# Kernel optimization log

Measured on AMD Instinct MI355X. Metric: run time of the kernel, lower is better.

The kernel has to match this reference:

```python
import jax, jax.numpy as jnp
import numpy as np

PC_RANGE = (-50.0, -50.0, -4.0, 50.0, 50.0, 4.0)
IMG_H, IMG_W = 256.0, 704.0
EPS = 1e-5


def _bilinear_sample(feat, u, v):
    # feat [H,W,C]; u,v [M] in [0,1]; matches F.grid_sample(align_corners=False, padding_mode='zeros')
    H, W, _ = feat.shape
    x = u * W - 0.5
    y = v * H - 0.5
    x0 = jnp.floor(x)
    y0 = jnp.floor(y)
    dx = (x - x0)[:, None]
    dy = (y - y0)[:, None]
    x0 = x0.astype(jnp.int32)
    y0 = y0.astype(jnp.int32)

    def g(xi, yi):
        inb = ((xi >= 0) & (xi < W) & (yi >= 0) & (yi < H)).astype(feat.dtype)[:, None]
        return feat[jnp.clip(yi, 0, H - 1), jnp.clip(xi, 0, W - 1)] * inb

    return (g(x0, y0) * (1 - dx) * (1 - dy) + g(x0 + 1, y0) * dx * (1 - dy)
            + g(x0, y0 + 1) * (1 - dx) * dy + g(x0 + 1, y0 + 1) * dx * dy)


def _conv1x1(t, w, b):
    return jnp.einsum('bchw,oc->bohw', t, w) + b[None, :, None, None]


def _inorm(t, eps=1e-5):
    # InstanceNorm2d (affine=False): normalize per (b, c) over spatial dims
    m = t.mean(axis=(2, 3), keepdims=True)
    var = t.var(axis=(2, 3), keepdims=True)
    return (t - m) * jax.lax.rsqrt(var + eps)


def _forward(feat, lidar2img, bev_pos, pe_w1, pe_b1, pe_w2, pe_b2, pe_w3, pe_b3,
             c1_w, c1_b, c2_w, c2_b, c3_w, c3_b):
    B, N, C, Hf, Wf = feat.shape
    _, P, Hb, Wb, _ = bev_pos.shape
    Q = Hb * Wb
    lo = jnp.asarray(PC_RANGE[:3], feat.dtype)
    hi = jnp.asarray(PC_RANGE[3:], feat.dtype)
    # 'b p h w d -> b (h w) p d', then scale normalized coords into pc_range
    ref01 = jnp.transpose(bev_pos, (0, 2, 3, 1, 4)).reshape(B, Q, P, 3)
    ref = ref01 * (hi - lo) + lo
    # project through per-camera lidar2img (homogeneous)
    pts = jnp.concatenate([ref, jnp.ones_like(ref[..., :1])], axis=-1)  # [B,Q,P,4]
    cam = jnp.einsum('bnij,bqpj->bnqpi', lidar2img, pts)                # [B,N,Q,P,4]
    homo = cam[..., 2]
    z = jnp.maximum(homo, EPS)
    u = cam[..., 0] / z / IMG_W
    v = cam[..., 1] / z / IMG_H
    valid = ((homo > EPS) & (u > 0.0) & (u < 1.0) & (v > 0.0) & (v < 1.0)).astype(feat.dtype)
    # bilinear gather per camera; feats to channel-last ('b n (g c) h w -> (b g) n h w c', G=1)
    fmap = jnp.transpose(feat, (0, 1, 3, 4, 2)).reshape(B * N, Hf, Wf, C)
    samp = jax.vmap(_bilinear_sample)(fmap, u.reshape(B * N, Q * P), v.reshape(B * N, Q * P))
    samp = samp.reshape(B, N, Q, P, C) * valid[..., None]
    samp = samp.sum(axis=1)  # sum over cameras -> [B,Q,P,C]
    # PositionalEncodingMap(3 -> 256 -> 256 -> 128) on normalized reference points
    pe = jax.nn.relu(ref01 @ pe_w1 + pe_b1)
    pe = jax.nn.relu(pe @ pe_w2 + pe_b2)
    pe = pe @ pe_w3 + pe_b3
    samp = samp + pe
    # 'b (h w) g p c -> b (p g c) h w' with g=1
    x = jnp.transpose(samp.reshape(B, Hb, Wb, P, C), (0, 3, 4, 1, 2)).reshape(B, P * C, Hb, Wb)
    gelu = lambda t: jax.nn.gelu(t, approximate=False)
    x = gelu(_inorm(_conv1x1(x, c1_w, c1_b)))
    x = gelu(_inorm(_conv1x1(x, c2_w, c2_b)))
    x = _conv1x1(x, c3_w, c3_b)
    return x


def setup_inputs() -> dict:
    key = jax.random.key(0)
    ks = jax.random.split(key, 16)
    B, N, C, Hf, Wf = 1, 6, 128, 32, 88
    P, Hb, Wb = 4, 160, 160
    E = 128
    MID = 256
    s = 0.02
    return {
        'feat': jax.random.normal(ks[0], (B, N, C, Hf, Wf), jnp.float32),
        'lidar2img': jax.random.normal(ks[1], (B, N, 4, 4), jnp.float32),
        'bev_pos': jax.random.uniform(ks[2], (B, P, Hb, Wb, 3), jnp.float32),
        'pe_w1': jax.random.normal(ks[3], (3, MID), jnp.float32) * s,
        'pe_b1': jnp.zeros((MID,), jnp.float32),
        'pe_w2': jax.random.normal(ks[4], (MID, MID), jnp.float32) * s,
        'pe_b2': jnp.zeros((MID,), jnp.float32),
        'pe_w3': jax.random.normal(ks[5], (MID, E), jnp.float32) * s,
        'pe_b3': jnp.zeros((E,), jnp.float32),
        'c1_w': jax.random.normal(ks[6], (4 * E, P * 128), jnp.float32) * s,
        'c1_b': jnp.zeros((4 * E,), jnp.float32),
        'c2_w': jax.random.normal(ks[7], (E, 4 * E), jnp.float32) * s,
        'c2_b': jnp.zeros((E,), jnp.float32),
        'c3_w': jax.random.normal(ks[8], (E, E), jnp.float32) * s,
        'c3_b': jnp.zeros((E,), jnp.float32),
    }


def reference(feat, lidar2img, bev_pos, pe_w1, pe_b1, pe_w2, pe_b2, pe_w3, pe_b3,
              c1_w, c1_b, c2_w, c2_b, c3_w, c3_b):
    return _forward(feat, lidar2img, bev_pos, pe_w1, pe_b1, pe_w2, pe_b2, pe_w3, pe_b3,
                    c1_w, c1_b, c2_w, c2_b, c3_w, c3_b)
```

## Files before the change

### kernel.cpp

```cpp
#include <hip/hip_runtime.h>
#include <cstdint>
#include <cstddef>

using frag8 = __attribute__((ext_vector_type(8))) short;
using f32x4 = __attribute__((ext_vector_type(4))) float;

__device__ __forceinline__ float b2f_bits(unsigned short u) {
    union { uint32_t u32; float f; } x; x.u32 = ((uint32_t)u) << 16; return x.f;
}
__device__ __forceinline__ float b2f_lo(uint32_t pk) {
    return __builtin_bit_cast(float, pk << 16);
}
__device__ __forceinline__ float b2f_hi(uint32_t pk) {
    return __builtin_bit_cast(float, pk & 0xffff0000u);
}
__device__ __forceinline__ unsigned short f2b(float f) {
    uint32_t u = __builtin_bit_cast(uint32_t, f);
    uint32_t r = (u + 0x7fffu + ((u >> 16) & 1u)) >> 16;
    return (unsigned short)r;
}

#define HF 32
#define WFEAT 88
#define NCAM 6
#define NPT 102400
#define BM 128
#define BN 128
#define BK 64

__global__ void k_transpose_feat(const float* __restrict__ feat,
                                 unsigned short* __restrict__ featT) {
    int idx = blockIdx.x * 256 + threadIdx.x;
    if (idx >= NCAM * 128 * HF * WFEAT) return;
    int c = idx & 127;
    int rest = idx >> 7;
    int x = rest % WFEAT; rest /= WFEAT;
    int y = rest % HF;
    int n = rest / HF;
    featT[idx] = f2b(feat[((n * 128 + c) * HF + y) * WFEAT + x]);
}

__global__ void k_transpose_w(const float* __restrict__ w,
                              unsigned short* __restrict__ wt, int R, int C) {
    int idx = blockIdx.x * 256 + threadIdx.x;
    if (idx >= R * C) return;
    int r = idx / C, c = idx - r * C;
    wt[c * R + r] = f2b(w[idx]);
}

__global__ void k_cast(const float* __restrict__ w, unsigned short* __restrict__ wb, int n) {
    int idx = blockIdx.x * 256 + threadIdx.x;
    if (idx < n) wb[idx] = f2b(w[idx]);
}

__global__ __launch_bounds__(256) void k_project(const float* __restrict__ l2i,
                                                 const float* __restrict__ bev,
                                                 int* __restrict__ poff,
                                                 float4* __restrict__ pwts) {
    int idx = blockIdx.x * 256 + threadIdx.x;
    if (idx >= NCAM * NPT) return;
    int n = idx / NPT, pt = idx - n * NPT;
    int q = pt >> 2, p = pt & 3;
    int h = q / 160, w = q - h * 160;
    const float* bv = bev + ((p * 160 + h) * 160 + w) * 3;
    float rx = bv[0] * 100.f - 50.f;
    float ry = bv[1] * 100.f - 50.f;
    float rz = bv[2] * 8.f - 4.f;
    const float* M = l2i + n * 16;
    float c0   = M[0] * rx + M[1] * ry + M[2]  * rz + M[3];
    float c1v  = M[4] * rx + M[5] * ry + M[6]  * rz + M[7];
    float homo = M[8] * rx + M[9] * ry + M[10] * rz + M[11];
    float z = fmaxf(homo, 1e-5f);
    float u = c0 / z / 704.0f;
    float v = c1v / z / 256.0f;
    if (!(homo > 1e-5f && u > 0.f && u < 1.f && v > 0.f && v < 1.f)) {
        poff[idx] = -1;
        return;
    }
    float fx = u * (float)WFEAT - 0.5f;
    float fy = v * (float)HF - 0.5f;
    float fx0 = floorf(fx), fy0 = floorf(fy);
    float dx = fx - fx0, dy = fy - fy0;
    int x0 = (int)fx0, y0 = (int)fy0;
    float wxa = (x0 < 0) ? dx : 1.f - dx;
    float wxb = (x0 >= 0 && x0 < WFEAT - 1) ? dx : 0.f;
    float wya = (y0 < 0) ? dy : 1.f - dy;
    float wyb = (y0 >= 0 && y0 < HF - 1) ? dy : 0.f;
    int bx = max(x0, 0), by = max(y0, 0);
    poff[idx] = ((n * HF + by) * WFEAT + bx) << 7;
    pwts[idx] = make_float4(wxa * wya, wxb * wya, wxa * wyb, wxb * wyb);
}

__global__ __launch_bounds__(256) void k_sample2(const unsigned short* __restrict__ featT,
                                                 const int* __restrict__ poff,
                                                 const float4* __restrict__ pwts,
                                                 unsigned short* __restrict__ samp) {
    int pt = blockIdx.x * 4 + (threadIdx.x >> 6);
    int lane = threadIdx.x & 63;
    int c2 = lane * 2;
    int offs[NCAM];
    float4 ww[NCAM];
    #pragma unroll
    for (int n = 0; n < NCAM; ++n) offs[n] = poff[n * NPT + pt];
    #pragma unroll
    for (int n = 0; n < NCAM; ++n) ww[n] = pwts[n * NPT + pt];
    float acc0 = 0.f, acc1 = 0.f;
    #pragma unroll
    for (int n = 0; n < NCAM; ++n) {
        if (offs[n] >= 0) {
            const unsigned short* base = featT + offs[n] + c2;
            uint32_t p00 = *(const uint32_t*)(base);
            uint32_t p01 = *(const uint32_t*)(base + 128);
            uint32_t p10 = *(const uint32_t*)(base + WFEAT * 128);
            uint32_t p11 = *(const uint32_t*)(base + WFEAT * 128 + 128);
            float4 w = ww[n];
            acc0 += w.x * b2f_lo(p00) + w.y * b2f_lo(p01) + w.z * b2f_lo(p10) + w.w * b2f_lo(p11);
            acc1 += w.x * b2f_hi(p00) + w.y * b2f_hi(p01) + w.z * b2f_hi(p10) + w.w * b2f_hi(p11);
        }
    }
    uint32_t outpk = (uint32_t)f2b(acc0) | ((uint32_t)f2b(acc1) << 16);
    *(uint32_t*)(samp + (size_t)pt * 128 + c2) = outpk;
}

__global__ __launch_bounds__(256) void k_pe1(const float* __restrict__ bev,
                                             const float* __restrict__ w1,
                                             const float* __restrict__ b1,
                                             unsigned short* __restrict__ H1) {
    int idx = blockIdx.x * 256 + threadIdx.x;
    int m = idx >> 6;
    int o4 = (idx & 63) * 4;
    int q = m >> 2, p = m & 3;
    int h = q / 160, w = q - h * 160;
    const float* bv = bev + ((p * 160 + h) * 160 + w) * 3;
    float cx = bv[0], cy = bv[1], cz = bv[2];
    float4 a0 = *(const float4*)(w1 + o4);
    float4 a1 = *(const float4*)(w1 + 256 + o4);
    float4 a2 = *(const float4*)(w1 + 512 + o4);
    float4 bb = *(const float4*)(b1 + o4);
    ushort4 o;
    o.x = f2b(fmaxf(cx * a0.x + cy * a1.x + cz * a2.x + bb.x, 0.f));
    o.y = f2b(fmaxf(cx * a0.y + cy * a1.y + cz * a2.y + bb.y, 0.f));
    o.z = f2b(fmaxf(cx * a0.z + cy * a1.z + cz * a2.z + bb.z, 0.f));
    o.w = f2b(fmaxf(cx * a0.w + cy * a1.w + cz * a2.w + bb.w, 0.f));
    *(ushort4*)(H1 + (size_t)m * 256 + o4) = o;
}

__device__ __forceinline__ void stage_tile_big(const unsigned short* __restrict__ g, int ld,
                                               unsigned short* lds, int t) {
    int r = t >> 2, cs = t & 3;
    int cl = cs ^ ((r >> 1) & 3);
    __builtin_amdgcn_global_load_lds(
        (const __attribute__((address_space(1))) void*)(g + (size_t)r * ld + cl * 8),
        (__attribute__((address_space(3))) void*)(lds + (t >> 6) * 512),
        16, 0, 0);
}

__device__ __forceinline__ frag8 frag_read_big(const unsigned short* lds, int row, int chunk) {
    return *(const frag8*)(lds + row * 32 + ((chunk ^ ((row >> 1) & 3)) << 3));
}

__device__ __forceinline__ void mma_tile_big(const unsigned short* As, const unsigned short* Bs,
                                             int wm, int wn, int lane, f32x4 (&acc)[4][4]) {
    int lm = lane & 15, lq = lane >> 4;
    frag8 a[4], b[4];
    #pragma unroll
    for (int t = 0; t < 4; ++t) a[t] = frag_read_big(As, wm * 64 + t * 16 + lm, lq);
    #pragma unroll
    for (int t = 0; t < 4; ++t) b[t] = frag_read_big(Bs, wn * 64 + t * 16 + lm, lq);
    #pragma unroll
    for (int tm = 0; tm < 4; ++tm)
        #pragma unroll
        for (int tn = 0; tn < 4; ++tn)
            acc[tm][tn] = __builtin_amdgcn_mfma_f32_16x16x32_bf16(a[tm], b[tn], acc[tm][tn], 0, 0, 0);
}

template <int KT>
__device__ __forceinline__ void gemm_loop_big(const unsigned short* __restrict__ A, int ldA,
                                              const unsigned short* __restrict__ B, int ldB,
                                              unsigned short (*As)[256 * 32],
                                              unsigned short (*Bs)[256 * 32],
                                              int t, int wm, int wn, int lane,
                                              f32x4 (&acc)[4][4]) {
    stage_tile_big(A, ldA, As[0], t);
    stage_tile_big(B, ldB, Bs[0], t);
    __syncthreads();
    #pragma unroll
    for (int kt = 0; kt < KT; ++kt) {
        int cur = kt & 1, nxt = cur ^ 1;
        if (kt + 1 < KT) {
            stage_tile_big(A + (kt + 1) * 32, ldA, As[nxt], t);
            stage_tile_big(B + (kt + 1) * 32, ldB, Bs[nxt], t);
        }
        mma_tile_big(As[cur], Bs[cur], wm, wn, lane, acc);
        __syncthreads();
    }
}

__global__ __launch_bounds__(1024) void k_gemm_pe2_big(const unsigned short* __restrict__ A,
                                                       const unsigned short* __restrict__ Bt,
                                                       const float* __restrict__ bias,
                                                       unsigned short* __restrict__ H2) {
    __shared__ unsigned short As[2][256 * 32], Bs[2][256 * 32];
    int t = threadIdx.x, lane = t & 63, wid = t >> 6;
    int wm = wid >> 2, wn = wid & 3;
    int m0 = blockIdx.x * 256;
    f32x4 acc[4][4] = {};
    gemm_loop_big<8>(A + (size_t)m0 * 256, 256, Bt, 256, As, Bs, t, wm, wn, lane, acc);
    int lm = lane & 15, lq = lane >> 4;
    #pragma unroll
    for (int tn = 0; tn < 4; ++tn) {
        int n = wn * 64 + tn * 16 + lm;
        float bn = bias[n];
        #pragma unroll
        for (int tm = 0; tm < 4; ++tm) {
            int mb = m0 + wm * 64 + tm * 16 + lq * 4;
            #pragma unroll
            for (int rr = 0; rr < 4; ++rr)
                H2[(size_t)(mb + rr) * 256 + n] = f2b(fmaxf(acc[tm][tn][rr] + bn, 0.f));
        }
    }
}

__global__ __launch_bounds__(1024) void k_gemm_conv1_big(const unsigned short* __restrict__ A,
                                                         const unsigned short* __restrict__ Bt,
                                                         const float* __restrict__ bias,
                                                         unsigned short* __restrict__ Y,
                                                         float* __restrict__ st) {
    __shared__ unsigned short As[2][256 * 32], Bs[2][256 * 32];
    int t = threadIdx.x, lane = t & 63, wid = t >> 6;
    int wm = wid >> 2, wn = wid & 3;
    int m0 = blockIdx.x * 256, n0 = blockIdx.y * 256;
    f32x4 acc[4][4] = {};
    gemm_loop_big<16>(A + (size_t)m0 * 512, 512, Bt + (size_t)n0 * 512, 512,
                      As, Bs, t, wm, wn, lane, acc);
    int lm = lane & 15, lq = lane >> 4;
    #pragma unroll
    for (int tn = 0; tn < 4; ++tn) {
        int n = n0 + wn * 64 + tn * 16 + lm;
        float bn = bias[n];
        float s1 = 0.f, s2 = 0.f;
        #pragma unroll
        for (int tm = 0; tm < 4; ++tm) {
            int mb = m0 + wm * 64 + tm * 16 + lq * 4;
            #pragma unroll
            for (int rr = 0; rr < 4; ++rr) {
                float v = acc[tm][tn][rr] + bn;
                Y[(size_t)(mb + rr) * 512 + n] = f2b(v);
                s1 += v; s2 += v * v;
            }
        }
        s1 += __shfl_xor(s1, 16); s1 += __shfl_xor(s1, 32);
        s2 += __shfl_xor(s2, 16); s2 += __shfl_xor(s2, 32);
        if (lq == 0) { atomicAdd(&st[n], s1); atomicAdd(&st[512 + n], s2); }
    }
}

__device__ __forceinline__ void stage_tile(const unsigned short* __restrict__ g, int ld,
                                           unsigned short* lds, int wave, int lane) {
    #pragma unroll
    for (int j = 0; j < 4; ++j) {
        int idx = wave * 256 + j * 64 + lane;
        int r = idx >> 3;
        int cs = idx & 7;
        int cl = cs ^ (r & 7);
        __builtin_amdgcn_global_load_lds(
            (const __attribute__((address_space(1))) void*)(g + (size_t)r * ld + cl * 8),
            (__attribute__((address_space(3))) void*)(lds + wave * 2048 + j * 512),
            16, 0, 0);
    }
}

__device__ __forceinline__ frag8 frag_read(const unsigned short* lds, int row, int chunk) {
    return *(const frag8*)(lds + row * 64 + ((chunk ^ (row & 7)) << 3));
}

__device__ __forceinline__ void mma_tile(const unsigned short* As, const unsigned short* Bs,
                                         int wm, int wn, int lane, f32x4 (&acc)[4][4]) {
    int lm = lane & 15, lq = lane >> 4;
    #pragma unroll
    for (int kk = 0; kk < 2; ++kk) {
        frag8 a[4], b[4];
        #pragma unroll
        for (int t = 0; t < 4; ++t) a[t] = frag_read(As, wm * 64 + t * 16 + lm, kk * 4 + lq);
        #pragma unroll
        for (int t = 0; t < 4; ++t) b[t] = frag_read(Bs, wn * 64 + t * 16 + lm, kk * 4 + lq);
        #pragma unroll
        for (int tm = 0; tm < 4; ++tm)
            #pragma unroll
            for (int tn = 0; tn < 4; ++tn)
                acc[tm][tn] = __builtin_amdgcn_mfma_f32_16x16x32_bf16(a[tm], b[tn], acc[tm][tn], 0, 0, 0);
    }
}

__global__ __launch_bounds__(256) void k_gemm_pe3(const unsigned short* __restrict__ A,
                                                  const unsigned short* __restrict__ Bt,
                                                  const float* __restrict__ bias,
                                                  const unsigned short* __restrict__ samp,
                                                  unsigned short* __restrict__ X) {
    __shared__ unsigned short As[BM * BK], Bs[BN * BK];
    int lane = threadIdx.x & 63, wave = threadIdx.x >> 6;
    int wm = wave >> 1, wn = wave & 1;
    int m0 = blockIdx.x * BM;
    f32x4 acc[4][4] = {};
    for (int kt = 0; kt < 4; ++kt) {
        stage_tile(A + (size_t)m0 * 256 + kt * BK, 256, As, wave, lane);
        stage_tile(Bt + (size_t)kt * BK, 256, Bs, wave, lane);
        __syncthreads();
        mma_tile(As, Bs, wm, wn, lane, acc);
        __syncthreads();
    }
    int lm = lane & 15, lq = lane >> 4;
    #pragma unroll
    for (int tn = 0; tn < 4; ++tn) {
        int n = wn * 64 + tn * 16 + lm;
        float bn = bias[n];
        #pragma unroll
        for (int tm = 0; tm < 4; ++tm) {
            int mb = m0 + wm * 64 + tm * 16 + lq * 4;
            #pragma unroll
            for (int rr = 0; rr < 4; ++rr) {
                size_t off = (size_t)(mb + rr) * 128 + n;
                X[off] = f2b(acc[tm][tn][rr] + bn + b2f_bits(samp[off]));
            }
        }
    }
}

template <int K, bool STATS>
__global__ __launch_bounds__(256) void k_gemm_conv(const unsigned short* __restrict__ A,
                                                   const unsigned short* __restrict__ Bt,
                                                   const float* __restrict__ bias,
                                                   unsigned short* __restrict__ Y, int ldY,
                                                   float* __restrict__ st, int C) {
    __shared__ unsigned short As[BM * BK], Bs[BN * BK];
    int lane = threadIdx.x & 63, wave = threadIdx.x >> 6;
    int wm = wave >> 1, wn = wave & 1;
    int m0 = blockIdx.x * BM, n0 = blockIdx.y * BN;
    f32x4 acc[4][4] = {};
    for (int kt = 0; kt < K / BK; ++kt) {
        stage_tile(A + (size_t)m0 * K + kt * BK, K, As, wave, lane);
        stage_tile(Bt + (size_t)n0 * K + kt * BK, K, Bs, wave, lane);
        __syncthreads();
        mma_tile(As, Bs, wm, wn, lane, acc);
        __syncthreads();
    }
    int lm = lane & 15, lq = lane >> 4;
    #pragma unroll
    for (int tn = 0; tn < 4; ++tn) {
        int n = n0 + wn * 64 + tn * 16 + lm;
        float bn = bias[n];
        float s1 = 0.f, s2 = 0.f;
        #pragma unroll
        for (int tm = 0; tm < 4; ++tm) {
            int mb = m0 + wm * 64 + tm * 16 + lq * 4;
            #pragma unroll
            for (int rr = 0; rr < 4; ++rr) {
                float v = acc[tm][tn][rr] + bn;
                Y[(size_t)(mb + rr) * ldY + n] = f2b(v);
                if (STATS) { s1 += v; s2 += v * v; }
            }
        }
        if (STATS) {
            s1 += __shfl_xor(s1, 16); s1 += __shfl_xor(s1, 32);
            s2 += __shfl_xor(s2, 16); s2 += __shfl_xor(s2, 32);
            if (lq == 0) { atomicAdd(&st[n], s1); atomicAdd(&st[C + n], s2); }
        }
    }
}

__global__ __launch_bounds__(256) void k_gemm_conv3(const unsigned short* __restrict__ A,
                                                    const unsigned short* __restrict__ Bt,
                                                    const float* __restrict__ bias,
                                                    float* __restrict__ out) {
    __shared__ unsigned short As[BM * BK], Bs[BN * BK];
    int lane = threadIdx.x & 63, wave = threadIdx.x >> 6;
    int wm = wave >> 1, wn = wave & 1;
    int m0 = blockIdx.x * BM;
    f32x4 acc[4][4] = {};
    for (int kt = 0; kt < 2; ++kt) {
        stage_tile(A + (size_t)m0 * 128 + kt * BK, 128, As, wave, lane);
        stage_tile(Bt + (size_t)kt * BK, 128, Bs, wave, lane);
        __syncthreads();
        mma_tile(As, Bs, wm, wn, lane, acc);
        __syncthreads();
    }
    int lm = lane & 15, lq = lane >> 4;
    #pragma unroll
    for (int tn = 0; tn < 4; ++tn) {
        int n = wn * 64 + tn * 16 + lm;
        float bn = bias[n];
        #pragma unroll
        for (int tm = 0; tm < 4; ++tm) {
            int mb = m0 + wm * 64 + tm * 16 + lq * 4;
            float4 pk;
            pk.x = acc[tm][tn][0] + bn;
            pk.y = acc[tm][tn][1] + bn;
            pk.z = acc[tm][tn][2] + bn;
            pk.w = acc[tm][tn][3] + bn;
            *(float4*)(out + (size_t)n * 25600 + mb) = pk;
        }
    }
}

__global__ void k_finalize(const float* __restrict__ st, float* __restrict__ ms,
                           int C, float inv_n) {
    int c = blockIdx.x * 256 + threadIdx.x;
    if (c >= C) return;
    float mean = st[c] * inv_n;
    float var = st[C + c] * inv_n - mean * mean;
    ms[c] = mean;
    ms[C + c] = rsqrtf(var + 1e-5f);
}

__global__ void k_normgelu8(const unsigned short* __restrict__ Y, const float* __restrict__ ms,
                            unsigned short* __restrict__ X2, int Cmask, int C, int total8) {
    int i8 = blockIdx.x * 256 + threadIdx.x;
    if (i8 >= total8) return;
    int e0 = i8 * 8;
    int c = e0 & Cmask;
    uint4 y = *(const uint4*)(Y + e0);
    const float is2 = 0.70710678118654752f;
    unsigned int yw[4] = {y.x, y.y, y.z, y.w};
    unsigned int ow[4];
    #pragma unroll
    for (int j = 0; j < 4; ++j) {
        float2 mu = *(const float2*)(ms + c + j * 2);
        float2 rs = *(const float2*)(ms + C + c + j * 2);
        float v0 = (b2f_bits((unsigned short)(yw[j] & 0xffffu)) - mu.x) * rs.x;
        float v1 = (b2f_bits((unsigned short)(yw[j] >> 16)) - mu.y) * rs.y;
        float g0 = 0.5f * v0 * (1.f + erff(v0 * is2));
        float g1 = 0.5f * v1 * (1.f + erff(v1 * is2));
        ow[j] = (uint32_t)f2b(g0) | ((uint32_t)f2b(g1) << 16);
    }
    *(uint4*)(X2 + e0) = make_uint4(ow[0], ow[1], ow[2], ow[3]);
}

extern "C" void kernel_launch(void* const* d_in, const int* in_sizes, int n_in,
                              void* d_out, int out_size, void* d_ws, size_t ws_size,
                              hipStream_t stream) {
    (void)in_sizes; (void)n_in; (void)out_size; (void)ws_size;
    const float* feat = (const float*)d_in[0];
    const float* l2i  = (const float*)d_in[1];
    const float* bev  = (const float*)d_in[2];
    const float* pw1  = (const float*)d_in[3];
    const float* pb1  = (const float*)d_in[4];
    const float* pw2  = (const float*)d_in[5];
    const float* pb2  = (const float*)d_in[6];
    const float* pw3  = (const float*)d_in[7];
    const float* pb3  = (const float*)d_in[8];
    const float* c1w  = (const float*)d_in[9];
    const float* c1b  = (const float*)d_in[10];
    const float* c2w  = (const float*)d_in[11];
    const float* c2b  = (const float*)d_in[12];
    const float* c3w  = (const float*)d_in[13];
    const float* c3b  = (const float*)d_in[14];
    float* outp = (float*)d_out;
    char* ws = (char*)d_ws;

    unsigned short* featT = (unsigned short*)(ws + 0);
    unsigned short* W2Tb  = (unsigned short*)(ws + 4348416);
    unsigned short* W3Tb  = (unsigned short*)(ws + 4479488);
    unsigned short* C1Wb  = (unsigned short*)(ws + 4545024);
    unsigned short* C2Wb  = (unsigned short*)(ws + 5069312);
    unsigned short* C3Wb  = (unsigned short*)(ws + 5200384);
    float* stats          = (float*)(ws + 5233152);
    int*    poff          = (int*)(ws + 5243392);
    float4* pwts          = (float4*)(ws + 7700992);
    char* BUF1 = ws + 17531392;
    char* BUF2 = ws + 69960192;
    char* BUF3 = ws + 122388992;

    float* st512 = stats;
    float* ms512 = stats + 1024;
    float* st128 = stats + 2048;
    float* ms128 = stats + 2304;

    unsigned short* H1   = (unsigned short*)BUF1;
    unsigned short* H2   = (unsigned short*)BUF2;
    unsigned short* samp = (unsigned short*)BUF3;
    unsigned short* X    = (unsigned short*)BUF1;
    unsigned short* Y1   = (unsigned short*)BUF2;
    unsigned short* X2   = (unsigned short*)BUF3;
    unsigned short* Y2   = (unsigned short*)BUF1;
    unsigned short* X3   = (unsigned short*)(BUF1 + 6553600);

    k_transpose_feat<<<8448, 256, 0, stream>>>(feat, featT);
    k_transpose_w<<<256, 256, 0, stream>>>(pw2, W2Tb, 256, 256);
    k_transpose_w<<<128, 256, 0, stream>>>(pw3, W3Tb, 256, 128);
    k_cast<<<1024, 256, 0, stream>>>(c1w, C1Wb, 262144);
    k_cast<<<256, 256, 0, stream>>>(c2w, C2Wb, 65536);
    k_cast<<<64, 256, 0, stream>>>(c3w, C3Wb, 16384);
    hipMemsetAsync(stats, 0, 10240, stream);

    k_project<<<2400, 256, 0, stream>>>(l2i, bev, poff, pwts);
    k_sample2<<<25600, 256, 0, stream>>>(featT, poff, pwts, samp);

    k_pe1<<<25600, 256, 0, stream>>>(bev, pw1, pb1, H1);
    k_gemm_pe2_big<<<400, 1024, 0, stream>>>(H1, W2Tb, pb2, H2);
    k_gemm_pe3<<<dim3(800, 1), 256, 0, stream>>>(H2, W3Tb, pb3, samp, X);

    k_gemm_conv1_big<<<dim3(100, 2), 1024, 0, stream>>>(X, C1Wb, c1b, Y1, st512);
    k_finalize<<<2, 256, 0, stream>>>(st512, ms512, 512, 1.f / 25600.f);
    k_normgelu8<<<6400, 256, 0, stream>>>(Y1, ms512, X2, 511, 512, 1638400);

    k_gemm_conv<512, true><<<dim3(200, 1), 256, 0, stream>>>(X2, C2Wb, c2b, Y2, 128, st128, 128);
    k_finalize<<<1, 256, 0, stream>>>(st128, ms128, 128, 1.f / 25600.f);
    k_normgelu8<<<1600, 256, 0, stream>>>(Y2, ms128, X3, 127, 128, 409600);

    k_gemm_conv3<<<dim3(200, 1), 256, 0, stream>>>(X3, C3Wb, c3b, outp);
}
```

Measured before the change: 297.7 us.

## Fuse prep kernels, compute PE layer-1 inside PE2 GEMM, fold finalize into norm-GELU

Merges the feature transpose, weight casts/transposes and camera projection into a single prep launch. Removes the separate PE layer-1 kernel and its bf16 H1 buffer by computing the first MLP layer on the fly while staging the A tile of the PE2 GEMM. Drops the two stats-finalize kernels by computing mean and rsqrt inside the norm-GELU kernel. This cuts launches and global memory traffic, at the cost of redundant per-thread stats math and extra ALU work in the GEMM staging path.

```diff
diff --git a/kernel.cpp b/kernel.cpp
--- a/kernel.cpp
+++ b/kernel.cpp
@@ -28,67 +28,95 @@
 #define BN 128
 #define BK 64
 
-__global__ void k_transpose_feat(const float* __restrict__ feat,
-                                 unsigned short* __restrict__ featT) {
-    int idx = blockIdx.x * 256 + threadIdx.x;
-    if (idx >= NCAM * 128 * HF * WFEAT) return;
-    int c = idx & 127;
-    int rest = idx >> 7;
-    int x = rest % WFEAT; rest /= WFEAT;
-    int y = rest % HF;
-    int n = rest / HF;
-    featT[idx] = f2b(feat[((n * 128 + c) * HF + y) * WFEAT + x]);
-}
-
-__global__ void k_transpose_w(const float* __restrict__ w,
-                              unsigned short* __restrict__ wt, int R, int C) {
-    int idx = blockIdx.x * 256 + threadIdx.x;
-    if (idx >= R * C) return;
-    int r = idx / C, c = idx - r * C;
-    wt[c * R + r] = f2b(w[idx]);
-}
-
-__global__ void k_cast(const float* __restrict__ w, unsigned short* __restrict__ wb, int n) {
-    int idx = blockIdx.x * 256 + threadIdx.x;
-    if (idx < n) wb[idx] = f2b(w[idx]);
-}
-
-__global__ __launch_bounds__(256) void k_project(const float* __restrict__ l2i,
-                                                 const float* __restrict__ bev,
-                                                 int* __restrict__ poff,
-                                                 float4* __restrict__ pwts) {
-    int idx = blockIdx.x * 256 + threadIdx.x;
-    if (idx >= NCAM * NPT) return;
-    int n = idx / NPT, pt = idx - n * NPT;
-    int q = pt >> 2, p = pt & 3;
-    int h = q / 160, w = q - h * 160;
-    const float* bv = bev + ((p * 160 + h) * 160 + w) * 3;
-    float rx = bv[0] * 100.f - 50.f;
-    float ry = bv[1] * 100.f - 50.f;
-    float rz = bv[2] * 8.f - 4.f;
-    const float* M = l2i + n * 16;
-    float c0   = M[0] * rx + M[1] * ry + M[2]  * rz + M[3];
-    float c1v  = M[4] * rx + M[5] * ry + M[6]  * rz + M[7];
-    float homo = M[8] * rx + M[9] * ry + M[10] * rz + M[11];
-    float z = fmaxf(homo, 1e-5f);
-    float u = c0 / z / 704.0f;
-    float v = c1v / z / 256.0f;
-    if (!(homo > 1e-5f && u > 0.f && u < 1.f && v > 0.f && v < 1.f)) {
-        poff[idx] = -1;
+__global__ __launch_bounds__(256) void k_prep(const float* __restrict__ feat,
+                                              const float* __restrict__ pw2,
+                                              const float* __restrict__ pw3,
+                                              const float* __restrict__ c1w,
+                                              const float* __restrict__ c2w,
+                                              const float* __restrict__ c3w,
+                                              const float* __restrict__ pw1,
+                                              const float* __restrict__ pb1,
+                                              const float* __restrict__ l2i,
+                                              const float* __restrict__ bev,
+                                              unsigned short* __restrict__ featT,
+                                              unsigned short* __restrict__ W2Tb,
+                                              unsigned short* __restrict__ W3Tb,
+                                              unsigned short* __restrict__ C1Wb,
+                                              unsigned short* __restrict__ C2Wb,
+                                              unsigned short* __restrict__ C3Wb,
+                                              float* __restrict__ w1p,
+                                              int* __restrict__ poff,
+                                              float4* __restrict__ pwts) {
+    int b = blockIdx.x, t = threadIdx.x;
+    if (b < 2400) {
+        int idx = b * 256 + t;
+        int n = idx / NPT, pt = idx - n * NPT;
+        int q = pt >> 2, p = pt & 3;
+        int h = q / 160, w = q - h * 160;
+        const float* bv = bev + ((p * 160 + h) * 160 + w) * 3;
+        float rx = bv[0] * 100.f - 50.f;
+        float ry = bv[1] * 100.f - 50.f;
+        float rz = bv[2] * 8.f - 4.f;
+        const float* M = l2i + n * 16;
+        float c0   = M[0] * rx + M[1] * ry + M[2]  * rz + M[3];
+        float c1v  = M[4] * rx + M[5] * ry + M[6]  * rz + M[7];
+        float homo = M[8] * rx + M[9] * ry + M[10] * rz + M[11];
+        float z = fmaxf(homo, 1e-5f);
+        float u = c0 / z / 704.0f;
+        float v = c1v / z / 256.0f;
+        if (!(homo > 1e-5f && u > 0.f && u < 1.f && v > 0.f && v < 1.f)) {
+            poff[idx] = -1;
+            return;
+        }
+        float fx = u * (float)WFEAT - 0.5f;
+        float fy = v * (float)HF - 0.5f;
+        float fx0 = floorf(fx), fy0 = floorf(fy);
+        float dx = fx - fx0, dy = fy - fy0;
+        int x0 = (int)fx0, y0 = (int)fy0;
+        float wxa = (x0 < 0) ? dx : 1.f - dx;
+        float wxb = (x0 >= 0 && x0 < WFEAT - 1) ? dx : 0.f;
+        float wya = (y0 < 0) ? dy : 1.f - dy;
+        float wyb = (y0 >= 0 && y0 < HF - 1) ? dy : 0.f;
+        int bx = max(x0, 0), by = max(y0, 0);
+        poff[idx] = ((n * HF + by) * WFEAT + bx) << 7;
+        pwts[idx] = make_float4(wxa * wya, wxb * wya, wxa * wyb, wxb * wyb);
         return;
     }
-    float fx = u * (float)WFEAT - 0.5f;
-    float fy = v * (float)HF - 0.5f;
-    float fx0 = floorf(fx), fy0 = floorf(fy);
-    float dx = fx - fx0, dy = fy - fy0;
-    int x0 = (int)fx0, y0 = (int)fy0;
-    float wxa = (x0 < 0) ? dx : 1.f - dx;
-    float wxb = (x0 >= 0 && x0 < WFEAT - 1) ? dx : 0.f;
-    float wya = (y0 < 0) ? dy : 1.f - dy;
-    float wyb = (y0 >= 0 && y0 < HF - 1) ? dy : 0.f;
-    int bx = max(x0, 0), by = max(y0, 0);
-    poff[idx] = ((n * HF + by) * WFEAT + bx) << 7;
-    pwts[idx] = make_float4(wxa * wya, wxb * wya, wxa * wyb, wxb * wyb);
+    b -= 2400;
+    if (b < 8448) {
+        int idx = b * 256 + t;
+        int c = idx & 127;
+        int rest = idx >> 7;
+        int x = rest % WFEAT; rest /= WFEAT;
+        int y = rest % HF;
+        int n = rest / HF;
+        featT[idx] = f2b(feat[((n * 128 + c) * HF + y) * WFEAT + x]);
+        return;
+    }
+    b -= 8448;
+    if (b < 256) {
+        int idx = b * 256 + t;
+        int r = idx >> 8, c = idx & 255;
+        W2Tb[c * 256 + r] = f2b(pw2[idx]);
+        return;
+    }
+    b -= 256;
+    if (b < 128) {
+        int idx = b * 256 + t;
+        int r = idx >> 7, c = idx & 127;
+        W3Tb[c * 256 + r] = f2b(pw3[idx]);
+        return;
+    }
+    b -= 128;
+    if (b < 1024) { int idx = b * 256 + t; C1Wb[idx] = f2b(c1w[idx]); return; }
+    b -= 1024;
+    if (b < 256)  { int idx = b * 256 + t; C2Wb[idx] = f2b(c2w[idx]); return; }
+    b -= 256;
+    if (b < 64)   { int idx = b * 256 + t; C3Wb[idx] = f2b(c3w[idx]); return; }
+    w1p[t * 4 + 0] = pw1[t];
+    w1p[t * 4 + 1] = pw1[256 + t];
+    w1p[t * 4 + 2] = pw1[512 + t];
+    w1p[t * 4 + 3] = pb1[t];
 }
 
 __global__ __launch_bounds__(256) void k_sample2(const unsigned short* __restrict__ featT,
@@ -122,29 +150,6 @@
     *(uint32_t*)(samp + (size_t)pt * 128 + c2) = outpk;
 }
 
-__global__ __launch_bounds__(256) void k_pe1(const float* __restrict__ bev,
-                                             const float* __restrict__ w1,
-                                             const float* __restrict__ b1,
-                                             unsigned short* __restrict__ H1) {
-    int idx = blockIdx.x * 256 + threadIdx.x;
-    int m = idx >> 6;
-    int o4 = (idx & 63) * 4;
-    int q = m >> 2, p = m & 3;
-    int h = q / 160, w = q - h * 160;
-    const float* bv = bev + ((p * 160 + h) * 160 + w) * 3;
-    float cx = bv[0], cy = bv[1], cz = bv[2];
-    float4 a0 = *(const float4*)(w1 + o4);
-    float4 a1 = *(const float4*)(w1 + 256 + o4);
-    float4 a2 = *(const float4*)(w1 + 512 + o4);
-    float4 bb = *(const float4*)(b1 + o4);
-    ushort4 o;
-    o.x = f2b(fmaxf(cx * a0.x + cy * a1.x + cz * a2.x + bb.x, 0.f));
-    o.y = f2b(fmaxf(cx * a0.y + cy * a1.y + cz * a2.y + bb.y, 0.f));
-    o.z = f2b(fmaxf(cx * a0.z + cy * a1.z + cz * a2.z + bb.z, 0.f));
-    o.w = f2b(fmaxf(cx * a0.w + cy * a1.w + cz * a2.w + bb.w, 0.f));
-    *(ushort4*)(H1 + (size_t)m * 256 + o4) = o;
-}
-
 __device__ __forceinline__ void stage_tile_big(const unsigned short* __restrict__ g, int ld,
                                                unsigned short* lds, int t) {
     int r = t >> 2, cs = t & 3;
@@ -172,6 +177,70 @@
         #pragma unroll
         for (int tn = 0; tn < 4; ++tn)
             acc[tm][tn] = __builtin_amdgcn_mfma_f32_16x16x32_bf16(a[tm], b[tn], acc[tm][tn], 0, 0, 0);
+}
+
+__global__ __launch_bounds__(1024) void k_gemm_pe2f(const float* __restrict__ bev,
+                                                    const float* __restrict__ w1p,
+                                                    const unsigned short* __restrict__ Bt,
+                                                    const float* __restrict__ bias,
+                                                    unsigned short* __restrict__ H2) {
+    __shared__ unsigned short As[2][256 * 32], Bs[2][256 * 32];
+    int t = threadIdx.x, lane = t & 63, wid = t >> 6;
+    int wm = wid >> 2, wn = wid & 3;
+    int m0 = blockIdx.x * 256;
+    int r = t >> 2, cs = t & 3;
+    int cl = cs ^ ((r >> 1) & 3);
+    int m = m0 + r;
+    int q = m >> 2, p = m & 3;
+    int h = q / 160, w = q - h * 160;
+    const float* bv = bev + ((p * 160 + h) * 160 + w) * 3;
+    float cx = bv[0], cy = bv[1], cz = bv[2];
+
+    f32x4 acc[4][4] = {};
+    {
+        int o = cl * 8;
+        union { unsigned short u[8]; frag8 v; } pk;
+        #pragma unroll
+        for (int j = 0; j < 8; ++j) {
+            float4 wv = *(const float4*)(w1p + (o + j) * 4);
+            float a = fmaf(cx, wv.x, fmaf(cy, wv.y, fmaf(cz, wv.z, wv.w)));
+            pk.u[j] = f2b(fmaxf(a, 0.f));
+        }
+        *(frag8*)(&As[0][r * 32 + cs * 8]) = pk.v;
+    }
+    stage_tile_big(Bt, 256, Bs[0], t);
+    __syncthreads();
+    #pragma unroll
+    for (int kt = 0; kt < 8; ++kt) {
+        int cur = kt & 1, nxt = cur ^ 1;
+        if (kt + 1 < 8) {
+            int o = (kt + 1) * 32 + cl * 8;
+            union { unsigned short u[8]; frag8 v; } pk;
+            #pragma unroll
+            for (int j = 0; j < 8; ++j) {
+                float4 wv = *(const float4*)(w1p + (o + j) * 4);
+                float a = fmaf(cx, wv.x, fmaf(cy, wv.y, fmaf(cz, wv.z, wv.w)));
+                pk.u[j] = f2b(fmaxf(a, 0.f));
+            }
+            *(frag8*)(&As[nxt][r * 32 + cs * 8]) = pk.v;
+            stage_tile_big(Bt + (kt + 1) * 32, 256, Bs[nxt], t);
+        }
+        mma_tile_big(As[cur], Bs[cur], wm, wn, lane, acc);
+        __syncthreads();
+    }
+    int lm = lane & 15, lq = lane >> 4;
+    #pragma unroll
+    for (int tn = 0; tn < 4; ++tn) {
+        int n = wn * 64 + tn * 16 + lm;
+        float bn = bias[n];
+        #pragma unroll
+        for (int tm = 0; tm < 4; ++tm) {
+            int mb = m0 + wm * 64 + tm * 16 + lq * 4;
+            #pragma unroll
+            for (int rr = 0; rr < 4; ++rr)
+                H2[(size_t)(mb + rr) * 256 + n] = f2b(fmaxf(acc[tm][tn][rr] + bn, 0.f));
+        }
+    }
 }
 
 template <int KT>
@@ -193,31 +262,6 @@
         }
         mma_tile_big(As[cur], Bs[cur], wm, wn, lane, acc);
         __syncthreads();
-    }
-}
-
-__global__ __launch_bounds__(1024) void k_gemm_pe2_big(const unsigned short* __restrict__ A,
-                                                       const unsigned short* __restrict__ Bt,
-                                                       const float* __restrict__ bias,
-                                                       unsigned short* __restrict__ H2) {
-    __shared__ unsigned short As[2][256 * 32], Bs[2][256 * 32];
-    int t = threadIdx.x, lane = t & 63, wid = t >> 6;
-    int wm = wid >> 2, wn = wid & 3;
-    int m0 = blockIdx.x * 256;
-    f32x4 acc[4][4] = {};
-    gemm_loop_big<8>(A + (size_t)m0 * 256, 256, Bt, 256, As, Bs, t, wm, wn, lane, acc);
-    int lm = lane & 15, lq = lane >> 4;
-    #pragma unroll
-    for (int tn = 0; tn < 4; ++tn) {
-        int n = wn * 64 + tn * 16 + lm;
-        float bn = bias[n];
-        #pragma unroll
-        for (int tm = 0; tm < 4; ++tm) {
-            int mb = m0 + wm * 64 + tm * 16 + lq * 4;
-            #pragma unroll
-            for (int rr = 0; rr < 4; ++rr)
-                H2[(size_t)(mb + rr) * 256 + n] = f2b(fmaxf(acc[tm][tn][rr] + bn, 0.f));
-        }
     }
 }
 
@@ -402,32 +446,31 @@
     }
 }
 
-__global__ void k_finalize(const float* __restrict__ st, float* __restrict__ ms,
-                           int C, float inv_n) {
-    int c = blockIdx.x * 256 + threadIdx.x;
-    if (c >= C) return;
-    float mean = st[c] * inv_n;
-    float var = st[C + c] * inv_n - mean * mean;
-    ms[c] = mean;
-    ms[C + c] = rsqrtf(var + 1e-5f);
-}
-
-__global__ void k_normgelu8(const unsigned short* __restrict__ Y, const float* __restrict__ ms,
-                            unsigned short* __restrict__ X2, int Cmask, int C, int total8) {
+__global__ void k_normgelu8f(const unsigned short* __restrict__ Y, const float* __restrict__ st,
+                             unsigned short* __restrict__ X2, int Cmask, int C, float inv_n,
+                             int total8) {
     int i8 = blockIdx.x * 256 + threadIdx.x;
     if (i8 >= total8) return;
     int e0 = i8 * 8;
     int c = e0 & Cmask;
     uint4 y = *(const uint4*)(Y + e0);
+    float4 s1a = *(const float4*)(st + c);
+    float4 s1b = *(const float4*)(st + c + 4);
+    float4 s2a = *(const float4*)(st + C + c);
+    float4 s2b = *(const float4*)(st + C + c + 4);
+    float mu[8] = { s1a.x * inv_n, s1a.y * inv_n, s1a.z * inv_n, s1a.w * inv_n,
+                    s1b.x * inv_n, s1b.y * inv_n, s1b.z * inv_n, s1b.w * inv_n };
+    float sq[8] = { s2a.x, s2a.y, s2a.z, s2a.w, s2b.x, s2b.y, s2b.z, s2b.w };
+    float rs[8];
+    #pragma unroll
+    for (int j = 0; j < 8; ++j) rs[j] = rsqrtf(sq[j] * inv_n - mu[j] * mu[j] + 1e-5f);
     const float is2 = 0.70710678118654752f;
     unsigned int yw[4] = {y.x, y.y, y.z, y.w};
     unsigned int ow[4];
     #pragma unroll
     for (int j = 0; j < 4; ++j) {
-        float2 mu = *(const float2*)(ms + c + j * 2);
-        float2 rs = *(const float2*)(ms + C + c + j * 2);
-        float v0 = (b2f_bits((unsigned short)(yw[j] & 0xffffu)) - mu.x) * rs.x;
-        float v1 = (b2f_bits((unsigned short)(yw[j] >> 16)) - mu.y) * rs.y;
+        float v0 = (b2f_bits((unsigned short)(yw[j] & 0xffffu)) - mu[j * 2]) * rs[j * 2];
+        float v1 = (b2f_bits((unsigned short)(yw[j] >> 16)) - mu[j * 2 + 1]) * rs[j * 2 + 1];
         float g0 = 0.5f * v0 * (1.f + erff(v0 * is2));
         float g1 = 0.5f * v1 * (1.f + erff(v1 * is2));
         ow[j] = (uint32_t)f2b(g0) | ((uint32_t)f2b(g1) << 16);
@@ -464,18 +507,16 @@
     unsigned short* C2Wb  = (unsigned short*)(ws + 5069312);
     unsigned short* C3Wb  = (unsigned short*)(ws + 5200384);
     float* stats          = (float*)(ws + 5233152);
-    int*    poff          = (int*)(ws + 5243392);
-    float4* pwts          = (float4*)(ws + 7700992);
-    char* BUF1 = ws + 17531392;
-    char* BUF2 = ws + 69960192;
-    char* BUF3 = ws + 122388992;
+    float* w1p            = (float*)(ws + 5243392);
+    int*    poff          = (int*)(ws + 5247488);
+    float4* pwts          = (float4*)(ws + 7705088);
+    char* BUF1 = ws + 17535488;
+    char* BUF2 = ws + 69964288;
+    char* BUF3 = ws + 122393088;
 
     float* st512 = stats;
-    float* ms512 = stats + 1024;
     float* st128 = stats + 2048;
-    float* ms128 = stats + 2304;
-
-    unsigned short* H1   = (unsigned short*)BUF1;
+
     unsigned short* H2   = (unsigned short*)BUF2;
     unsigned short* samp = (unsigned short*)BUF3;
     unsigned short* X    = (unsigned short*)BUF1;
@@ -484,28 +525,20 @@
     unsigned short* Y2   = (unsigned short*)BUF1;
     unsigned short* X3   = (unsigned short*)(BUF1 + 6553600);
 
-    k_transpose_feat<<<8448, 256, 0, stream>>>(feat, featT);
-    k_transpose_w<<<256, 256, 0, stream>>>(pw2, W2Tb, 256, 256);
-    k_transpose_w<<<128, 256, 0, stream>>>(pw3, W3Tb, 256, 128);
-    k_cast<<<1024, 256, 0, stream>>>(c1w, C1Wb, 262144);
-    k_cast<<<256, 256, 0, stream>>>(c2w, C2Wb, 65536);
-    k_cast<<<64, 256, 0, stream>>>(c3w, C3Wb, 16384);
     hipMemsetAsync(stats, 0, 10240, stream);
-
-    k_project<<<2400, 256, 0, stream>>>(l2i, bev, poff, pwts);
+    k_prep<<<12577, 256, 0, stream>>>(feat, pw2, pw3, c1w, c2w, c3w, pw1, pb1, l2i, bev,
+                                      featT, W2Tb, W3Tb, C1Wb, C2Wb, C3Wb, w1p, poff, pwts);
+
     k_sample2<<<25600, 256, 0, stream>>>(featT, poff, pwts, samp);
 
-    k_pe1<<<25600, 256, 0, stream>>>(bev, pw1, pb1, H1);
-    k_gemm_pe2_big<<<400, 1024, 0, stream>>>(H1, W2Tb, pb2, H2);
+    k_gemm_pe2f<<<400, 1024, 0, stream>>>(bev, w1p, W2Tb, pb2, H2);
     k_gemm_pe3<<<dim3(800, 1), 256, 0, stream>>>(H2, W3Tb, pb3, samp, X);
 
     k_gemm_conv1_big<<<dim3(100, 2), 1024, 0, stream>>>(X, C1Wb, c1b, Y1, st512);
-    k_finalize<<<2, 256, 0, stream>>>(st512, ms512, 512, 1.f / 25600.f);
-    k_normgelu8<<<6400, 256, 0, stream>>>(Y1, ms512, X2, 511, 512, 1638400);
+    k_normgelu8f<<<6400, 256, 0, stream>>>(Y1, st512, X2, 511, 512, 1.f / 25600.f, 1638400);
 
     k_gemm_conv<512, true><<<dim3(200, 1), 256, 0, stream>>>(X2, C2Wb, c2b, Y2, 128, st128, 128);
-    k_finalize<<<1, 256, 0, stream>>>(st128, ms128, 128, 1.f / 25600.f);
-    k_normgelu8<<<1600, 256, 0, stream>>>(Y2, ms128, X3, 127, 128, 409600);
+    k_normgelu8f<<<1600, 256, 0, stream>>>(Y2, st128, X3, 127, 128, 1.f / 25600.f, 409600);
 
     k_gemm_conv3<<<dim3(200, 1), 256, 0, stream>>>(X3, C3Wb, c3b, outp);
 }
```

New measurement: 324.6 us. +9.0%, slower.
